# Optimization experiments

Measured on AMD Instinct MI355X. Metric: run time of the kernel, lower is better.

Reference implementation:

```python
import jax, jax.numpy as jnp
import numpy as np

N_NODES = 100000
N_EDGES = 1600000
D_FEAT = 64      # per-node embedding dim; nin = 2*D_FEAT = 128
N_OUT = 64
NSLOPE = 0.2


def setup_inputs() -> dict:
    key = jax.random.key(0)
    k0, k1, k2, k3, k4, k5 = jax.random.split(key, 6)
    nodes = jax.random.normal(k0, (N_NODES, D_FEAT), dtype=jnp.float32)
    src = jax.random.randint(k1, (N_EDGES,), 0, N_NODES, dtype=jnp.int32)
    dst = jax.random.randint(k2, (N_EDGES,), 0, N_NODES, dtype=jnp.int32)
    # Linear(nin=2*D_FEAT, nout=N_OUT) weight/bias and Linear(nout,1,bias=False)
    W_w = jax.random.normal(k3, (N_OUT, 2 * D_FEAT), dtype=jnp.float32) * (2 * D_FEAT) ** -0.5
    W_b = jax.random.normal(k4, (N_OUT,), dtype=jnp.float32) * 0.02
    a_w = jax.random.normal(k5, (N_OUT,), dtype=jnp.float32) * N_OUT ** -0.5
    return {"nodes": nodes, "src": src, "dst": dst, "W_w": W_w, "W_b": W_b, "a_w": a_w}


def reference(nodes, src, dst, W_w, W_b, a_w):
    # Per edge: score = a( LeakyReLU( W [h_src ; h_dst] + b ) )
    # Split W over the concat so we project each node once, then gather.
    d = nodes.shape[1]
    W1, W2 = W_w[:, :d], W_w[:, d:]          # [nout, d] each
    p1 = nodes @ W1.T                        # [N, nout]
    p2 = nodes @ W2.T                        # [N, nout]
    hw = p1[src] + p2[dst] + W_b             # [E, nout]  (== W(cat(hi,hj)))
    act = jnp.where(hw >= 0, hw, NSLOPE * hw)  # LeakyReLU
    scores = act @ a_w                       # [E]
    # Sparse softmax over dim=1 of the [N,N] score matrix == segment softmax
    # over edges grouped by the row (src) index, numerically stabilized.
    n = nodes.shape[0]
    m = jax.ops.segment_max(scores, src, num_segments=n)   # [N]
    e = jnp.exp(scores - m[src])                            # [E]
    s = jax.ops.segment_sum(e, src, num_segments=n)         # [N]
    attn = e / s[src]                                       # [E]
    return attn
```

## Files before the change

kernel.cpp:

```cpp
#include <hip/hip_runtime.h>

#define NSLOPE 0.2f

static __device__ inline unsigned short f2bf(float f) {
    unsigned u = __float_as_uint(f);
    unsigned r = u + 0x7FFFu + ((u >> 16) & 1u);
    return (unsigned short)(r >> 16);
}
static __device__ inline unsigned pack2(float a, float b) {
    return (unsigned)f2bf(a) | ((unsigned)f2bf(b) << 16);
}
static __device__ inline float bflo(unsigned u) { return __uint_as_float(u << 16); }
static __device__ inline float bfhi(unsigned u) { return __uint_as_float(u & 0xFFFF0000u); }

#define PB_NODES 64
#define WT_STRIDE 132
#define NT_STRIDE 68

__global__ __launch_bounds__(256) void proj_kernel(
    const float* __restrict__ nodes, const float* __restrict__ Ww,
    const float* __restrict__ Wb,
    unsigned short* __restrict__ P1, unsigned short* __restrict__ P2,
    float* __restrict__ ssum, int nNodes)
{
    __shared__ float wT[64 * WT_STRIDE];
    __shared__ float nT[64 * NT_STRIDE];
    const int t = threadIdx.x;
    const int base = blockIdx.x * PB_NODES;

    if (t < PB_NODES) {
        int n = base + t;
        if (n < nNodes) ssum[n] = 0.f;
    }

    for (int idx = t; idx < 64 * 128; idx += 256) {
        int o = idx >> 7, c = idx & 127;
        float v = Ww[idx];
        int j, dd;
        if (c < 64) { j = o;      dd = c;      }
        else        { j = 64 + o; dd = c - 64; }
        wT[dd * WT_STRIDE + j] = v;
    }
    for (int f = t; f < PB_NODES * 16; f += 256) {
        int n = f >> 4;
        int dpos = (f & 15) * 4;
        float4 v = make_float4(0.f, 0.f, 0.f, 0.f);
        if (base + n < nNodes)
            v = *(const float4*)(nodes + (size_t)(base + n) * 64 + dpos);
        nT[(dpos + 0) * NT_STRIDE + n] = v.x;
        nT[(dpos + 1) * NT_STRIDE + n] = v.y;
        nT[(dpos + 2) * NT_STRIDE + n] = v.z;
        nT[(dpos + 3) * NT_STRIDE + n] = v.w;
    }
    __syncthreads();

    const int ng = t & 15;
    const int og = t >> 4;
    float acc[4][8];
    #pragma unroll
    for (int i = 0; i < 4; i++)
        #pragma unroll
        for (int j = 0; j < 8; j++) acc[i][j] = 0.f;

    #pragma unroll 4
    for (int d = 0; d < 64; ++d) {
        float4 nv = *(const float4*)&nT[d * NT_STRIDE + ng * 4];
        float4 w0 = *(const float4*)&wT[d * WT_STRIDE + og * 8];
        float4 w1 = *(const float4*)&wT[d * WT_STRIDE + og * 8 + 4];
        float nvv[4] = {nv.x, nv.y, nv.z, nv.w};
        float wv[8]  = {w0.x, w0.y, w0.z, w0.w, w1.x, w1.y, w1.z, w1.w};
        #pragma unroll
        for (int i = 0; i < 4; i++)
            #pragma unroll
            for (int j = 0; j < 8; j++)
                acc[i][j] = fmaf(nvv[i], wv[j], acc[i][j]);
    }

    const int joutbase = og * 8;
    float wb[8];
    if (og < 8) {
        #pragma unroll
        for (int j = 0; j < 8; j++) wb[j] = Wb[joutbase + j];
    }
    #pragma unroll
    for (int i = 0; i < 4; i++) {
        int n = base + ng * 4 + i;
        if (n < nNodes) {
            if (og < 8) {
                uint4 o;
                o.x = pack2(acc[i][0] + wb[0], acc[i][1] + wb[1]);
                o.y = pack2(acc[i][2] + wb[2], acc[i][3] + wb[3]);
                o.z = pack2(acc[i][4] + wb[4], acc[i][5] + wb[5]);
                o.w = pack2(acc[i][6] + wb[6], acc[i][7] + wb[7]);
                *(uint4*)(P1 + (size_t)n * 64 + joutbase) = o;
            } else {
                int jb = joutbase - 64;
                uint4 o;
                o.x = pack2(acc[i][0], acc[i][1]);
                o.y = pack2(acc[i][2], acc[i][3]);
                o.z = pack2(acc[i][4], acc[i][5]);
                o.w = pack2(acc[i][6], acc[i][7]);
                *(uint4*)(P2 + (size_t)n * 64 + jb) = o;
            }
        }
    }
}

__global__ __launch_bounds__(256) void edge_score_kernel(
    const unsigned short* __restrict__ P1, const unsigned short* __restrict__ P2,
    const int* __restrict__ src, const int* __restrict__ dst,
    const float* __restrict__ a_w,
    float* __restrict__ evals, float* __restrict__ ssum, int nE)
{
    int tid = blockIdx.x * 256 + threadIdx.x;
    int e   = tid >> 3;
    int sub = tid & 7;
    if (e >= nE) return;

    int s = src[e];
    int d = dst[e];
    uint4 r1 = *(const uint4*)(P1 + (size_t)s * 64 + sub * 8);
    uint4 r2 = *(const uint4*)(P2 + (size_t)d * 64 + sub * 8);
    float4 a0 = *(const float4*)(a_w + sub * 8);
    float4 a1 = *(const float4*)(a_w + sub * 8 + 4);

    float partial = 0.f, h;
    h = bflo(r1.x) + bflo(r2.x); h = (h >= 0.f) ? h : NSLOPE * h; partial = fmaf(h, a0.x, partial);
    h = bfhi(r1.x) + bfhi(r2.x); h = (h >= 0.f) ? h : NSLOPE * h; partial = fmaf(h, a0.y, partial);
    h = bflo(r1.y) + bflo(r2.y); h = (h >= 0.f) ? h : NSLOPE * h; partial = fmaf(h, a0.z, partial);
    h = bfhi(r1.y) + bfhi(r2.y); h = (h >= 0.f) ? h : NSLOPE * h; partial = fmaf(h, a0.w, partial);
    h = bflo(r1.z) + bflo(r2.z); h = (h >= 0.f) ? h : NSLOPE * h; partial = fmaf(h, a1.x, partial);
    h = bfhi(r1.z) + bfhi(r2.z); h = (h >= 0.f) ? h : NSLOPE * h; partial = fmaf(h, a1.y, partial);
    h = bflo(r1.w) + bflo(r2.w); h = (h >= 0.f) ? h : NSLOPE * h; partial = fmaf(h, a1.z, partial);
    h = bfhi(r1.w) + bfhi(r2.w); h = (h >= 0.f) ? h : NSLOPE * h; partial = fmaf(h, a1.w, partial);

    partial += __shfl_xor(partial, 1);
    partial += __shfl_xor(partial, 2);
    partial += __shfl_xor(partial, 4);

    if (sub == 0) {
        float ev = __expf(partial);
        evals[e] = ev;
        atomicAdd(&ssum[s], ev);
    }
}

__global__ __launch_bounds__(256) void normalize_kernel(
    const int* __restrict__ src, const float* __restrict__ ssum,
    float* __restrict__ out, int nE)
{
    int i = blockIdx.x * 256 + threadIdx.x;
    int e4 = i * 4;
    if (e4 + 3 < nE) {
        float4 ev = *(const float4*)(out + e4);
        int4   sv = *(const int4*)(src + e4);
        float4 r;
        r.x = ev.x / ssum[sv.x];
        r.y = ev.y / ssum[sv.y];
        r.z = ev.z / ssum[sv.z];
        r.w = ev.w / ssum[sv.w];
        *(float4*)(out + e4) = r;
    } else {
        for (int e = e4; e < nE; ++e) out[e] = out[e] / ssum[src[e]];
    }
}

extern "C" void kernel_launch(void* const* d_in, const int* in_sizes, int n_in,
                              void* d_out, int out_size, void* d_ws, size_t ws_size,
                              hipStream_t stream) {
    (void)n_in; (void)out_size; (void)ws_size;
    const float* nodes = (const float*)d_in[0];
    const int*   src   = (const int*)d_in[1];
    const int*   dst   = (const int*)d_in[2];
    const float* Ww    = (const float*)d_in[3];
    const float* Wb    = (const float*)d_in[4];
    const float* a_w   = (const float*)d_in[5];
    float* out = (float*)d_out;

    const int nNodes = in_sizes[0] / 64;
    const int nE     = in_sizes[1];

    unsigned short* P1   = (unsigned short*)d_ws;
    unsigned short* P2   = P1 + (size_t)nNodes * 64;
    float*          ssum = (float*)(P2 + (size_t)nNodes * 64);

    int nblocks_proj = (nNodes + PB_NODES - 1) / PB_NODES;
    proj_kernel<<<nblocks_proj, 256, 0, stream>>>(nodes, Ww, Wb, P1, P2, ssum, nNodes);

    int nblocks_edge = (int)(((long long)nE * 8 + 255) / 256);
    edge_score_kernel<<<nblocks_edge, 256, 0, stream>>>(P1, P2, src, dst, a_w, out, ssum, nE);

    int nthreads_norm = (nE + 3) / 4;
    int nblocks_norm  = (nthreads_norm + 255) / 256;
    normalize_kernel<<<nblocks_norm, 256, 0, stream>>>(src, ssum, out, nE);
}
```

Measured before the change: 132.8 us.

## Use bf16 MFMA for node projection, add reciprocal pass and nontemporal accesses

The node projection now runs on bf16 MFMA instructions. A small prep kernel converts and reorders the weights to bf16, and nodes are converted to bf16 in shared memory. A separate kernel precomputes 1/ssum per node so normalization multiplies instead of divides, and the edge and normalize kernels use nontemporal loads and stores for streaming data. In exchange it adds two kernel launches, rounds the node and weight inputs to bf16 before the matmul, and writes the projection output as scalar 2-byte stores instead of 16-byte vector stores.

```diff
diff --git a/kernel.cpp b/kernel.cpp
--- a/kernel.cpp
+++ b/kernel.cpp
@@ -1,106 +1,101 @@
 #include <hip/hip_runtime.h>
 
 #define NSLOPE 0.2f
+
+typedef __attribute__((ext_vector_type(8))) short short8;
+typedef __attribute__((ext_vector_type(4))) float floatx4;
+typedef __attribute__((ext_vector_type(4))) float f32x4;
+typedef __attribute__((ext_vector_type(4))) int   i32x4;
 
 static __device__ inline unsigned short f2bf(float f) {
     unsigned u = __float_as_uint(f);
     unsigned r = u + 0x7FFFu + ((u >> 16) & 1u);
     return (unsigned short)(r >> 16);
 }
-static __device__ inline unsigned pack2(float a, float b) {
-    return (unsigned)f2bf(a) | ((unsigned)f2bf(b) << 16);
-}
 static __device__ inline float bflo(unsigned u) { return __uint_as_float(u << 16); }
 static __device__ inline float bfhi(unsigned u) { return __uint_as_float(u & 0xFFFF0000u); }
 
-#define PB_NODES 64
-#define WT_STRIDE 132
-#define NT_STRIDE 68
-
-__global__ __launch_bounds__(256) void proj_kernel(
-    const float* __restrict__ nodes, const float* __restrict__ Ww,
+__global__ __launch_bounds__(256) void prep_kernel(const float* __restrict__ Ww,
+                                                   unsigned short* __restrict__ Wbf) {
+    int t = threadIdx.x;
+    for (int idx = t; idx < 64 * 128; idx += 256) {
+        int o = idx >> 7, c = idx & 127;
+        int j, k;
+        if (c < 64) { j = o;      k = c;      }
+        else        { j = 64 + o; k = c - 64; }
+        Wbf[j * 64 + k] = f2bf(Ww[idx]);
+    }
+}
+
+#define PNB 128
+#define AST 72
+
+__global__ __launch_bounds__(256) void proj_mfma_kernel(
+    const float* __restrict__ nodes, const unsigned short* __restrict__ Wbf,
     const float* __restrict__ Wb,
     unsigned short* __restrict__ P1, unsigned short* __restrict__ P2,
     float* __restrict__ ssum, int nNodes)
 {
-    __shared__ float wT[64 * WT_STRIDE];
-    __shared__ float nT[64 * NT_STRIDE];
+    __shared__ unsigned short aT[PNB * AST];
+    __shared__ unsigned short wT[128 * AST];
     const int t = threadIdx.x;
-    const int base = blockIdx.x * PB_NODES;
-
-    if (t < PB_NODES) {
-        int n = base + t;
-        if (n < nNodes) ssum[n] = 0.f;
-    }
-
-    for (int idx = t; idx < 64 * 128; idx += 256) {
-        int o = idx >> 7, c = idx & 127;
-        float v = Ww[idx];
-        int j, dd;
-        if (c < 64) { j = o;      dd = c;      }
-        else        { j = 64 + o; dd = c - 64; }
-        wT[dd * WT_STRIDE + j] = v;
-    }
-    for (int f = t; f < PB_NODES * 16; f += 256) {
-        int n = f >> 4;
-        int dpos = (f & 15) * 4;
+    const int base = blockIdx.x * PNB;
+
+    if (t < PNB) { int n = base + t; if (n < nNodes) ssum[n] = 0.f; }
+
+    for (int f = t; f < PNB * 16; f += 256) {
+        int n = f >> 4, dpos = (f & 15) * 4;
         float4 v = make_float4(0.f, 0.f, 0.f, 0.f);
-        if (base + n < nNodes)
-            v = *(const float4*)(nodes + (size_t)(base + n) * 64 + dpos);
-        nT[(dpos + 0) * NT_STRIDE + n] = v.x;
-        nT[(dpos + 1) * NT_STRIDE + n] = v.y;
-        nT[(dpos + 2) * NT_STRIDE + n] = v.z;
-        nT[(dpos + 3) * NT_STRIDE + n] = v.w;
+        if (base + n < nNodes) v = *(const float4*)(nodes + (size_t)(base + n) * 64 + dpos);
+        ushort4 o;
+        o.x = f2bf(v.x); o.y = f2bf(v.y); o.z = f2bf(v.z); o.w = f2bf(v.w);
+        *(ushort4*)&aT[n * AST + dpos] = o;
+    }
+    for (int i = t; i < 1024; i += 256) {
+        int j = i >> 3, koff = (i & 7) * 8;
+        uint4 v = *(const uint4*)(Wbf + j * 64 + koff);
+        *(uint4*)&wT[j * AST + koff] = v;
     }
     __syncthreads();
 
-    const int ng = t & 15;
-    const int og = t >> 4;
-    float acc[4][8];
+    const int w = t >> 6, lane = t & 63;
+    const int lr = lane & 15;
+    const int lk = (lane >> 4) * 8;
+
+    floatx4 acc[2][8];
     #pragma unroll
-    for (int i = 0; i < 4; i++)
+    for (int rt = 0; rt < 2; rt++)
         #pragma unroll
-        for (int j = 0; j < 8; j++) acc[i][j] = 0.f;
-
-    #pragma unroll 4
-    for (int d = 0; d < 64; ++d) {
-        float4 nv = *(const float4*)&nT[d * NT_STRIDE + ng * 4];
-        float4 w0 = *(const float4*)&wT[d * WT_STRIDE + og * 8];
-        float4 w1 = *(const float4*)&wT[d * WT_STRIDE + og * 8 + 4];
-        float nvv[4] = {nv.x, nv.y, nv.z, nv.w};
-        float wv[8]  = {w0.x, w0.y, w0.z, w0.w, w1.x, w1.y, w1.z, w1.w};
+        for (int ct = 0; ct < 8; ct++) acc[rt][ct] = (floatx4){0.f, 0.f, 0.f, 0.f};
+
+    #pragma unroll
+    for (int ks = 0; ks < 2; ks++) {
+        int k0 = ks * 32 + lk;
+        short8 a0 = *(const short8*)&aT[((w * 2 + 0) * 16 + lr) * AST + k0];
+        short8 a1 = *(const short8*)&aT[((w * 2 + 1) * 16 + lr) * AST + k0];
         #pragma unroll
-        for (int i = 0; i < 4; i++)
+        for (int ct = 0; ct < 8; ct++) {
+            short8 b = *(const short8*)&wT[(ct * 16 + lr) * AST + k0];
+            acc[0][ct] = __builtin_amdgcn_mfma_f32_16x16x32_bf16(a0, b, acc[0][ct], 0, 0, 0);
+            acc[1][ct] = __builtin_amdgcn_mfma_f32_16x16x32_bf16(a1, b, acc[1][ct], 0, 0, 0);
+        }
+    }
+
+    #pragma unroll
+    for (int ct = 0; ct < 8; ct++) {
+        int j = ct * 16 + lr;
+        float bias = (j < 64) ? Wb[j] : 0.f;
+        #pragma unroll
+        for (int rt = 0; rt < 2; rt++) {
             #pragma unroll
-            for (int j = 0; j < 8; j++)
-                acc[i][j] = fmaf(nvv[i], wv[j], acc[i][j]);
-    }
-
-    const int joutbase = og * 8;
-    float wb[8];
-    if (og < 8) {
-        #pragma unroll
-        for (int j = 0; j < 8; j++) wb[j] = Wb[joutbase + j];
-    }
-    #pragma unroll
-    for (int i = 0; i < 4; i++) {
-        int n = base + ng * 4 + i;
-        if (n < nNodes) {
-            if (og < 8) {
-                uint4 o;
-                o.x = pack2(acc[i][0] + wb[0], acc[i][1] + wb[1]);
-                o.y = pack2(acc[i][2] + wb[2], acc[i][3] + wb[3]);
-                o.z = pack2(acc[i][4] + wb[4], acc[i][5] + wb[5]);
-                o.w = pack2(acc[i][6] + wb[6], acc[i][7] + wb[7]);
-                *(uint4*)(P1 + (size_t)n * 64 + joutbase) = o;
-            } else {
-                int jb = joutbase - 64;
-                uint4 o;
-                o.x = pack2(acc[i][0], acc[i][1]);
-                o.y = pack2(acc[i][2], acc[i][3]);
-                o.z = pack2(acc[i][4], acc[i][5]);
-                o.w = pack2(acc[i][6], acc[i][7]);
-                *(uint4*)(P2 + (size_t)n * 64 + jb) = o;
+            for (int r = 0; r < 4; r++) {
+                int nl = (w * 2 + rt) * 16 + (lane >> 4) * 4 + r;
+                int n = base + nl;
+                if (n < nNodes) {
+                    unsigned short val = f2bf(acc[rt][ct][r] + bias);
+                    if (j < 64) P1[(size_t)n * 64 + j]      = val;
+                    else        P2[(size_t)n * 64 + j - 64] = val;
+                }
             }
         }
     }
@@ -117,8 +112,8 @@
     int sub = tid & 7;
     if (e >= nE) return;
 
-    int s = src[e];
-    int d = dst[e];
+    int s = __builtin_nontemporal_load(&src[e]);
+    int d = __builtin_nontemporal_load(&dst[e]);
     uint4 r1 = *(const uint4*)(P1 + (size_t)s * 64 + sub * 8);
     uint4 r2 = *(const uint4*)(P2 + (size_t)d * 64 + sub * 8);
     float4 a0 = *(const float4*)(a_w + sub * 8);
@@ -140,28 +135,34 @@
 
     if (sub == 0) {
         float ev = __expf(partial);
-        evals[e] = ev;
+        __builtin_nontemporal_store(ev, &evals[e]);
         atomicAdd(&ssum[s], ev);
     }
 }
 
+__global__ __launch_bounds__(256) void recip_kernel(const float* __restrict__ ssum,
+                                                    float* __restrict__ rinv, int nNodes) {
+    int n = blockIdx.x * 256 + threadIdx.x;
+    if (n < nNodes) rinv[n] = 1.0f / ssum[n];
+}
+
 __global__ __launch_bounds__(256) void normalize_kernel(
-    const int* __restrict__ src, const float* __restrict__ ssum,
+    const int* __restrict__ src, const float* __restrict__ rinv,
     float* __restrict__ out, int nE)
 {
     int i = blockIdx.x * 256 + threadIdx.x;
     int e4 = i * 4;
     if (e4 + 3 < nE) {
-        float4 ev = *(const float4*)(out + e4);
-        int4   sv = *(const int4*)(src + e4);
-        float4 r;
-        r.x = ev.x / ssum[sv.x];
-        r.y = ev.y / ssum[sv.y];
-        r.z = ev.z / ssum[sv.z];
-        r.w = ev.w / ssum[sv.w];
-        *(float4*)(out + e4) = r;
+        f32x4 ev = __builtin_nontemporal_load((const f32x4*)(out + e4));
+        i32x4 sv = __builtin_nontemporal_load((const i32x4*)(src + e4));
+        f32x4 r;
+        r.x = ev.x * rinv[sv.x];
+        r.y = ev.y * rinv[sv.y];
+        r.z = ev.z * rinv[sv.z];
+        r.w = ev.w * rinv[sv.w];
+        __builtin_nontemporal_store(r, (f32x4*)(out + e4));
     } else {
-        for (int e = e4; e < nE; ++e) out[e] = out[e] / ssum[src[e]];
+        for (int e = e4; e < nE; ++e) out[e] = out[e] * rinv[src[e]];
     }
 }
 
@@ -183,14 +184,21 @@
     unsigned short* P1   = (unsigned short*)d_ws;
     unsigned short* P2   = P1 + (size_t)nNodes * 64;
     float*          ssum = (float*)(P2 + (size_t)nNodes * 64);
-
-    int nblocks_proj = (nNodes + PB_NODES - 1) / PB_NODES;
-    proj_kernel<<<nblocks_proj, 256, 0, stream>>>(nodes, Ww, Wb, P1, P2, ssum, nNodes);
+    float*          rinv = ssum + nNodes;
+    unsigned short* Wbf  = (unsigned short*)(rinv + nNodes);
+
+    prep_kernel<<<1, 256, 0, stream>>>(Ww, Wbf);
+
+    int nblocks_proj = (nNodes + PNB - 1) / PNB;
+    proj_mfma_kernel<<<nblocks_proj, 256, 0, stream>>>(nodes, Wbf, Wb, P1, P2, ssum, nNodes);
 
     int nblocks_edge = (int)(((long long)nE * 8 + 255) / 256);
     edge_score_kernel<<<nblocks_edge, 256, 0, stream>>>(P1, P2, src, dst, a_w, out, ssum, nE);
 
+    int nblocks_recip = (nNodes + 255) / 256;
+    recip_kernel<<<nblocks_recip, 256, 0, stream>>>(ssum, rinv, nNodes);
+
     int nthreads_norm = (nE + 3) / 4;
     int nblocks_norm  = (nthreads_norm + 255) / 256;
-    normalize_kernel<<<nblocks_norm, 256, 0, stream>>>(src, ssum, out, nE);
-}
+    normalize_kernel<<<nblocks_norm, 256, 0, stream>>>(src, rinv, out, nE);
+}
```

Result: no change. 133.6 us (+0.6%).
